# Kernel tuning notes

Hardware: AMD Instinct MI355X
Metric: run time of the kernel (lower is better)

The kernel has to match this reference:

```python
import jax, jax.numpy as jnp
import numpy as np

H = 128
N = 100_000
VOCAB = 15_128
LAYER_TIMESTEPS = [5, 2, 5, 2]
RESIDUALS = {1: [0], 3: [1]}


def gru_cell(x, h, Wih, Whh, bih, bhh):
    # torch.nn.GRUCell semantics
    gi = x @ Wih.T + bih
    gh = h @ Whh.T + bhh
    ir, iz, inn = jnp.split(gi, 3, axis=-1)
    hr, hz, hn = jnp.split(gh, 3, axis=-1)
    r = jax.nn.sigmoid(ir + hr)
    z = jax.nn.sigmoid(iz + hz)
    n = jnp.tanh(inn + r * hn)
    return (1.0 - z) * n + z * h


def setup_inputs() -> dict:
    key = jax.random.key(0)
    ks = jax.random.split(key, 12)
    E_AST, E_MASTER, V, P = 100_000, 20_000, 30_000, 8_000
    s = 1.0 / np.sqrt(H)
    inp = {
        "node_type_ids": jax.random.randint(ks[0], (N,), 0, VOCAB),
        "edges_ast": jax.random.randint(ks[1], (E_AST, 2), 0, N),
        "edges_master": jax.random.randint(ks[2], (E_MASTER, 2), 0, N),
        "var_node_pos": jax.random.randint(ks[3], (V,), 0, N),
        "pred_node_ids": jax.random.randint(ks[4], (P,), 0, N),
        # learned params
        "embedding": jax.random.normal(ks[5], (VOCAB, H), jnp.float32) * 0.02,
        "msg_W": jax.random.normal(ks[6], (4, 4, H, H), jnp.float32) * s,  # [layer, edge_type, H, H]
        "msg_b": jnp.zeros((4, 4, H), jnp.float32),
        "Wih_a": jax.random.normal(ks[7], (2, 3 * H, H), jnp.float32) * s,      # GRU input weights, layers 0,2 (no residual)
        "Wih_b": jax.random.normal(ks[8], (2, 3 * H, 2 * H), jnp.float32) * s,  # layers 1,3 (one residual, concat -> 2H)
        "Whh": jax.random.normal(ks[9], (4, 3 * H, H), jnp.float32) * s,
        "bih": jnp.zeros((4, 3 * H), jnp.float32),
        "bhh": jnp.zeros((4, 3 * H), jnp.float32),
    }
    return inp


def reference(node_type_ids, edges_ast, edges_master, var_node_pos, pred_node_ids,
              embedding, msg_W, msg_b, Wih_a, Wih_b, Whh, bih, bhh):
    # initial node encodings via embedding lookup
    h = embedding[node_type_ids]  # [N, H]
    # 4 edge types: ast, reversed ast, var->master, master->var
    edge_lists = [edges_ast, edges_ast[:, ::-1], edges_master, edges_master[:, ::-1]]
    node_states = [h]
    num_nodes = h.shape[0]
    for layer in range(4):
        res_states = [node_states[l] for l in RESIDUALS.get(layer, [])]
        Wih = Wih_a[layer // 2] if layer in (0, 2) else Wih_b[layer // 2]
        for _ in range(LAYER_TIMESTEPS[layer]):
            incoming = jnp.zeros_like(h)
            for e, edges in enumerate(edge_lists):
                # gather source states, per-edge-type linear, scatter-add to targets
                msg = h[edges[:, 0]] @ msg_W[layer, e].T + msg_b[layer, e]
                incoming = incoming + jax.ops.segment_sum(msg, edges[:, 1], num_segments=num_nodes)
            x = jnp.concatenate([incoming] + res_states, axis=-1) if res_states else incoming
            h = gru_cell(x, h, Wih, Whh[layer], bih[layer], bhh[layer])
        node_states.append(h)
    tree_node_encoding = h
    packed_variable_encoding = tree_node_encoding[var_node_pos]
    prediction_node_encoding = tree_node_encoding[pred_node_ids]
    return tree_node_encoding, packed_variable_encoding, prediction_node_encoding
```

## Files before the change

kernel.cpp:

```cpp
#include <hip/hip_runtime.h>
#include <math.h>

#define H 128
#define NN 100000
#define E_AST 100000
#define E_MST 20000
#define E_TOT 240000
#define NV 30000
#define NP 8000
#define N4 400000
#define NH 12800000
#define VOCAB 15128

typedef unsigned short ushort_t;
typedef __attribute__((ext_vector_type(8))) unsigned short us8;
typedef _Float16 half8 __attribute__((ext_vector_type(8)));
typedef __attribute__((ext_vector_type(4))) float f32x4;

__device__ __forceinline__ unsigned short f2h(float f) {
    _Float16 h = (_Float16)f;
    return __builtin_bit_cast(unsigned short, h);
}
__device__ __forceinline__ float h2f(unsigned short u) {
    return (float)__builtin_bit_cast(_Float16, u);
}
__device__ __forceinline__ void fsplit(float x, unsigned short& hi, unsigned short& lo) {
    _Float16 a = (_Float16)x;
    _Float16 b = (_Float16)(x - (float)a);
    hi = __builtin_bit_cast(unsigned short, a);
    lo = __builtin_bit_cast(unsigned short, b);
}

#define GLD16(gsrc, ldst) __builtin_amdgcn_global_load_lds( \
    (const __attribute__((address_space(1))) unsigned int*)(gsrc), \
    (__attribute__((address_space(3))) unsigned int*)(ldst), 16, 0, 0)

__global__ void embed_kernel(const int* __restrict__ ids, const float* __restrict__ emb,
                             ushort_t* __restrict__ h16, ushort_t* __restrict__ hlo) {
    int g = blockIdx.x * 256 + threadIdx.x;
    if (g >= NN * 64) return;
    int i = g >> 6, j2 = (g & 63) << 1;
    float2 v = *(const float2*)&emb[(size_t)ids[i] * H + j2];
    unsigned short h0, l0, h1, l1;
    fsplit(v.x, h0, l0); fsplit(v.y, h1, l1);
    *(unsigned*)&h16[(size_t)i * H + j2] = (unsigned)h0 | ((unsigned)h1 << 16);
    *(unsigned*)&hlo[(size_t)i * H + j2] = (unsigned)l0 | ((unsigned)l1 << 16);
}

__device__ inline void edge_decode(int t, const int* __restrict__ ast, const int* __restrict__ mst,
                                   int& e, int& src, int& tgt) {
    if (t < E_AST)                 { e = 0; src = ast[2*t];     tgt = ast[2*t+1]; }
    else if (t < 2*E_AST)          { int i = t - E_AST;         e = 1; src = ast[2*i+1]; tgt = ast[2*i]; }
    else if (t < 2*E_AST + E_MST)  { int i = t - 2*E_AST;       e = 2; src = mst[2*i];   tgt = mst[2*i+1]; }
    else                           { int i = t - 2*E_AST-E_MST; e = 3; src = mst[2*i+1]; tgt = mst[2*i]; }
}

__global__ void count4_kernel(const int* __restrict__ ast, const int* __restrict__ mst,
                              int* __restrict__ deg4) {
    int t = blockIdx.x * 256 + threadIdx.x;
    if (t >= E_TOT) return;
    int e, src, tgt; edge_decode(t, ast, mst, e, src, tgt);
    atomicAdd(&deg4[tgt * 4 + e], 1);
}

__global__ void scan1b(const int* __restrict__ deg, int* __restrict__ excl,
                       int* __restrict__ partial, int n) {
    __shared__ int sm[256];
    int t = threadIdx.x, b = blockIdx.x;
    int base = b * 2048 + t * 8;
    int v[8]; int s = 0;
    #pragma unroll
    for (int i = 0; i < 8; ++i) { v[i] = (base + i < n) ? deg[base + i] : 0; s += v[i]; }
    sm[t] = s;
    __syncthreads();
    for (int off = 1; off < 256; off <<= 1) {
        int x = (t >= off) ? sm[t - off] : 0;
        __syncthreads();
        sm[t] += x;
        __syncthreads();
    }
    int run = sm[t] - s;
    if (t == 255) partial[b] = sm[255];
    #pragma unroll
    for (int i = 0; i < 8; ++i) {
        if (base + i < n) { excl[base + i] = run; run += v[i]; }
    }
}

__global__ void scan2(int* __restrict__ partial, int nb) {
    __shared__ int sm[256];
    int t = threadIdx.x;
    int v = (t < nb) ? partial[t] : 0;
    sm[t] = v;
    __syncthreads();
    for (int off = 1; off < 256; off <<= 1) {
        int x = (t >= off) ? sm[t - off] : 0;
        __syncthreads();
        sm[t] += x;
        __syncthreads();
    }
    if (t < nb) partial[t] = sm[t] - v;
}

__global__ void scan3b(int* __restrict__ rp, const int* __restrict__ partial, int n, int etot) {
    int i = blockIdx.x * 256 + threadIdx.x;
    if (i < n) rp[i] += partial[i >> 11];
    if (i == n) rp[n] = etot;
}

__global__ void fill4_kernel(const int* __restrict__ ast, const int* __restrict__ mst,
                             const int* __restrict__ rp4, int* __restrict__ cnt4,
                             int* __restrict__ col) {
    int t = blockIdx.x * 256 + threadIdx.x;
    if (t >= E_TOT) return;
    int e, src, tgt; edge_decode(t, ast, mst, e, src, tgt);
    int key = tgt * 4 + e;
    int slot = rp4[key] + atomicAdd(&cnt4[key], 1);
    col[slot] = src;
}

__global__ void prep_wmsg2(const float* __restrict__ W, ushort_t* __restrict__ hi,
                           ushort_t* __restrict__ lo) {
    int i = blockIdx.x * 256 + threadIdx.x;
    if (i >= 262144) return;
    fsplit(W[i], hi[i], lo[i]);
}

__global__ void prep_emb16(const float* __restrict__ emb, ushort_t* __restrict__ emb16) {
    int i = blockIdx.x * 256 + threadIdx.x;
    if (i >= VOCAB * H) return;
    emb16[i] = f2h(emb[i]);
}

__global__ void prep_B2(const float* __restrict__ Wih_a, const float* __restrict__ Wih_b,
                        const float* __restrict__ Whh,
                        ushort_t* __restrict__ B1h, ushort_t* __restrict__ B1l,
                        ushort_t* __restrict__ B2h, ushort_t* __restrict__ B2l) {
    int i = blockIdx.x * 256 + threadIdx.x;
    if (i >= 327680) return;
    int l, off, K;
    if (i < 65536)       { l = 0; off = 0;      K = 256; }
    else if (i < 163840) { l = 1; off = 65536;  K = 384; }
    else if (i < 229376) { l = 2; off = 163840; K = 256; }
    else                 { l = 3; off = 229376; K = 384; }
    int Kx = K - 128;
    const float* Wih = (l & 1) ? (Wih_b + (size_t)(l >> 1) * 384 * 256)
                               : (Wih_a + (size_t)(l >> 1) * 384 * 128);
    const float* WhhL = Whh + (size_t)l * 384 * 128;
    int rem = i - off;
    int row = rem / K, k = rem - row * K;
    int j = row >> 1, s = row & 1;
    int g1 = s * 128 + j;
    float v1 = (k < Kx) ? Wih[(size_t)g1 * Kx + k] : WhhL[(size_t)g1 * 128 + (k - Kx)];
    fsplit(v1, B1h[i], B1l[i]);
    int g2 = 256 + j;
    float v2;
    if (s == 0) v2 = (k < Kx) ? Wih[(size_t)g2 * Kx + k] : 0.f;
    else        v2 = (k < Kx) ? 0.f : WhhL[(size_t)g2 * 128 + (k - Kx)];
    fsplit(v2, B2h[i], B2l[i]);
}

__global__ __launch_bounds__(256, 4) void msg_gemm(
    const ushort_t* __restrict__ h16, const ushort_t* __restrict__ Whi,
    const ushort_t* __restrict__ Wlo, ushort_t* __restrict__ TA, ushort_t* __restrict__ TB)
{
    __shared__ ushort_t sh[16384];
    ushort_t* Ah = sh;
    ushort_t* Bs = sh + 8192;
    const int tid = threadIdx.x, w = tid >> 6, l = tid & 63;
    const int m0 = blockIdx.x * 128;
    const int n0 = blockIdx.y * 128;
    const int wm = w >> 1, wn = w & 1;
    const int lr8 = l >> 3, lslot = (l & 7) ^ lr8;
    f32x4 acc[4][4];
    #pragma unroll
    for (int a = 0; a < 4; ++a)
        #pragma unroll
        for (int b = 0; b < 4; ++b) acc[a][b] = (f32x4){0.f, 0.f, 0.f, 0.f};

    for (int kt = 0; kt < 2; ++kt) {
        const int kk = kt * 64;
        #pragma unroll
        for (int q = 0; q < 4; ++q) {
            int row8 = w * 4 + q;
            int grow = m0 + row8 * 8 + lr8; if (grow >= NN) grow = NN - 1;
            GLD16(h16 + (size_t)grow * H + kk + lslot * 8, Ah + row8 * 512);
        }
        #pragma unroll
        for (int q = 0; q < 4; ++q) {
            int row8 = w * 4 + q;
            GLD16(Whi + (size_t)(n0 + row8 * 8 + lr8) * 128 + kk + lslot * 8, Bs + row8 * 512);
        }
        __syncthreads();
        #pragma unroll
        for (int fk = 0; fk < 2; ++fk) {
            half8 av[4], bv[4];
            #pragma unroll
            for (int fm = 0; fm < 4; ++fm) {
                int row = wm * 64 + fm * 16 + (l & 15);
                int slot = (fk * 4 + (l >> 4)) ^ (row & 7);
                av[fm] = *(const half8*)&Ah[row * 64 + slot * 8];
            }
            #pragma unroll
            for (int fn = 0; fn < 4; ++fn) {
                int row = wn * 64 + fn * 16 + (l & 15);
                int slot = (fk * 4 + (l >> 4)) ^ (row & 7);
                bv[fn] = *(const half8*)&Bs[row * 64 + slot * 8];
            }
            #pragma unroll
            for (int fm = 0; fm < 4; ++fm)
                #pragma unroll
                for (int fn = 0; fn < 4; ++fn)
                    acc[fm][fn] = __builtin_amdgcn_mfma_f32_16x16x32_f16(av[fm], bv[fn], acc[fm][fn], 0, 0, 0);
        }
        __syncthreads();
        #pragma unroll
        for (int q = 0; q < 4; ++q) {
            int row8 = w * 4 + q;
            GLD16(Wlo + (size_t)(n0 + row8 * 8 + lr8) * 128 + kk + lslot * 8, Bs + row8 * 512);
        }
        __syncthreads();
        #pragma unroll
        for (int fk = 0; fk < 2; ++fk) {
            half8 av[4], bv[4];
            #pragma unroll
            for (int fm = 0; fm < 4; ++fm) {
                int row = wm * 64 + fm * 16 + (l & 15);
                int slot = (fk * 4 + (l >> 4)) ^ (row & 7);
                av[fm] = *(const half8*)&Ah[row * 64 + slot * 8];
            }
            #pragma unroll
            for (int fn = 0; fn < 4; ++fn) {
                int row = wn * 64 + fn * 16 + (l & 15);
                int slot = (fk * 4 + (l >> 4)) ^ (row & 7);
                bv[fn] = *(const half8*)&Bs[row * 64 + slot * 8];
            }
            #pragma unroll
            for (int fm = 0; fm < 4; ++fm)
                #pragma unroll
                for (int fn = 0; fn < 4; ++fn)
                    acc[fm][fn] = __builtin_amdgcn_mfma_f32_16x16x32_f16(av[fm], bv[fn], acc[fm][fn], 0, 0, 0);
        }
        __syncthreads();
    }
    #pragma unroll
    for (int fm = 0; fm < 4; ++fm)
        #pragma unroll
        for (int fn = 0; fn < 4; ++fn) {
            int colL = wn * 64 + fn * 16 + (l & 15);
            #pragma unroll
            for (int rg = 0; rg < 4; ++rg) {
                int rowL = wm * 64 + fm * 16 + (l >> 4) * 4 + rg;
                sh[rowL * 128 + colL] = f2h(acc[fm][fn][rg]);
            }
        }
    __syncthreads();
    {
        int row = tid >> 1, half = tid & 1;
        int grow = m0 + row;
        if (grow < NN) {
            ushort_t* dst = ((blockIdx.y < 2) ? TA : TB) + (size_t)grow * 256 + (blockIdx.y & 1) * 128 + half * 64;
            const ushort_t* src = &sh[row * 128 + half * 64];
            #pragma unroll
            for (int q = 0; q < 8; ++q)
                *(us8*)&dst[q * 8] = *(const us8*)&src[q * 8];
        }
    }
}

__global__ void gather_all(const ushort_t* __restrict__ TA, const ushort_t* __restrict__ TB,
                           const int* __restrict__ rp4, const int* __restrict__ col,
                           const int* __restrict__ deg4, const float* __restrict__ mb,
                           ushort_t* __restrict__ inc16) {
    int wv = threadIdx.x >> 6, l = threadIdx.x & 63;
    int t = blockIdx.x * 4 + wv;
    if (t >= NN) return;
    int c2 = l * 2;
    float a0 = 0.f, a1 = 0.f;
    #pragma unroll
    for (int e4 = 0; e4 < 4; ++e4) {
        float d = (float)deg4[t * 4 + e4];
        a0 += d * mb[e4 * H + c2];
        a1 += d * mb[e4 * H + c2 + 1];
    }
    #pragma unroll
    for (int e = 0; e < 4; ++e) {
        const ushort_t* Tb = (e < 2) ? TA : TB;
        int cb = (e & 1) * 128;
        int s0 = rp4[4 * t + e], s1 = rp4[4 * t + e + 1];
        for (int s = s0; s < s1; ++s) {
            unsigned vv = *(const unsigned*)&Tb[(size_t)col[s] * 256 + cb + c2];
            a0 += h2f((unsigned short)(vv & 0xffff));
            a1 += h2f((unsigned short)(vv >> 16));
        }
    }
    *(unsigned*)&inc16[(size_t)t * H + c2] = (unsigned)f2h(a0) | ((unsigned)f2h(a1) << 16);
}

template<int CFG>
__global__ __launch_bounds__(256, 3) void gru_fused(
    const ushort_t* __restrict__ inc16, ushort_t* __restrict__ h16, ushort_t* __restrict__ hlo,
    const ushort_t* __restrict__ s1h, const ushort_t* __restrict__ emb16, const int* __restrict__ ids,
    const ushort_t* __restrict__ B1h, const ushort_t* __restrict__ B1l,
    const ushort_t* __restrict__ B2h, const ushort_t* __restrict__ B2l,
    const float* __restrict__ bihL, const float* __restrict__ bhhL)
{
    constexpr int NPARTS = (CFG == 0) ? 2 : 3;
    constexpr int K = NPARTS * 128;
    __shared__ ushort_t sh[18432];
    ushort_t* Ah = sh;
    ushort_t* Bs = sh + 2048;
    const int tid = threadIdx.x, w = tid >> 6, l = tid & 63;
    const int m0 = blockIdx.x * 32;
    const int lr8 = l >> 3, lslot = (l & 7) ^ lr8;

    float rzr[2][4][4], rzz[2][4][4];
    f32x4 acc[2][4];

    #pragma unroll
    for (int pass = 0; pass < 2; ++pass) {
        const ushort_t* Bh = pass ? B2h : B1h;
        const ushort_t* Bl = pass ? B2l : B1l;
        #pragma unroll
        for (int a = 0; a < 2; ++a)
            #pragma unroll
            for (int b = 0; b < 4; ++b) acc[a][b] = (f32x4){0.f, 0.f, 0.f, 0.f};

        for (int kt = 0; kt < NPARTS * 2; ++kt) {
            const int p = kt >> 1;
            const int kk = (kt & 1) * 64;
            const int kb = p * 128 + kk;
            {
                int grow = m0 + w * 8 + lr8;
                const ushort_t* sb;
                if (p == 0)               sb = inc16 + (size_t)grow * H;
                else if (p == NPARTS - 1) sb = h16 + (size_t)grow * H;
                else if (CFG == 1)        sb = emb16 + (size_t)ids[grow] * H;
                else                      sb = s1h + (size_t)grow * H;
                GLD16(sb + kk + lslot * 8, Ah + w * 512);
            }
            #pragma unroll
            for (int q = 0; q < 8; ++q)
                GLD16(Bh + (size_t)((w * 8 + q) * 8 + lr8) * K + kb + lslot * 8, Bs + (w * 8 + q) * 512);
            __syncthreads();
            #pragma unroll
            for (int fk = 0; fk < 2; ++fk) {
                half8 av[2], bv[4];
                #pragma unroll
                for (int fm = 0; fm < 2; ++fm) {
                    int row = fm * 16 + (l & 15);
                    int slot = (fk * 4 + (l >> 4)) ^ (row & 7);
                    av[fm] = *(const half8*)&Ah[row * 64 + slot * 8];
                }
                #pragma unroll
                for (int fn = 0; fn < 4; ++fn) {
                    int row = w * 64 + fn * 16 + (l & 15);
                    int slot = (fk * 4 + (l >> 4)) ^ (row & 7);
                    bv[fn] = *(const half8*)&Bs[row * 64 + slot * 8];
                }
                #pragma unroll
                for (int fm = 0; fm < 2; ++fm)
                    #pragma unroll
                    for (int fn = 0; fn < 4; ++fn)
                        acc[fm][fn] = __builtin_amdgcn_mfma_f32_16x16x32_f16(av[fm], bv[fn], acc[fm][fn], 0, 0, 0);
            }
            __syncthreads();
            #pragma unroll
            for (int q = 0; q < 8; ++q)
                GLD16(Bl + (size_t)((w * 8 + q) * 8 + lr8) * K + kb + lslot * 8, Bs + (w * 8 + q) * 512);
            __syncthreads();
            #pragma unroll
            for (int fk = 0; fk < 2; ++fk) {
                half8 av[2], bv[4];
                #pragma unroll
                for (int fm = 0; fm < 2; ++fm) {
                    int row = fm * 16 + (l & 15);
                    int slot = (fk * 4 + (l >> 4)) ^ (row & 7);
                    av[fm] = *(const half8*)&Ah[row * 64 + slot * 8];
                }
                #pragma unroll
                for (int fn = 0; fn < 4; ++fn) {
                    int row = w * 64 + fn * 16 + (l & 15);
                    int slot = (fk * 4 + (l >> 4)) ^ (row & 7);
                    bv[fn] = *(const half8*)&Bs[row * 64 + slot * 8];
                }
                #pragma unroll
                for (int fm = 0; fm < 2; ++fm)
                    #pragma unroll
                    for (int fn = 0; fn < 4; ++fn)
                        acc[fm][fn] = __builtin_amdgcn_mfma_f32_16x16x32_f16(av[fm], bv[fn], acc[fm][fn], 0, 0, 0);
            }
            __syncthreads();
        }

        if (pass == 0) {
            #pragma unroll
            for (int fn = 0; fn < 4; ++fn) {
                int cc = w * 64 + fn * 16 + (l & 15);
                int j = cc >> 1, s = cc & 1;
                float bsum = s ? (bihL[128 + j] + bhhL[128 + j]) : (bihL[j] + bhhL[j]);
                #pragma unroll
                for (int fm = 0; fm < 2; ++fm)
                    #pragma unroll
                    for (int rg = 0; rg < 4; ++rg) {
                        float g = 1.f / (1.f + __expf(-(acc[fm][fn][rg] + bsum)));
                        float other = __shfl_xor(g, 1);
                        rzr[fm][fn][rg] = s ? other : g;
                        rzz[fm][fn][rg] = s ? g : other;
                    }
            }
        } else {
            ushort_t* ohi = Bs;
            ushort_t* olo = Bs + 4096;
            #pragma unroll
            for (int fn = 0; fn < 4; ++fn) {
                int cc = w * 64 + fn * 16 + (l & 15);
                int j = cc >> 1, s = cc & 1;
                float bsum = s ? bhhL[256 + j] : bihL[256 + j];
                #pragma unroll
                for (int fm = 0; fm < 2; ++fm)
                    #pragma unroll
                    for (int rg = 0; rg < 4; ++rg) {
                        float self = acc[fm][fn][rg] + bsum;
                        float other = __shfl_xor(self, 1);
                        if (s == 0) {
                            int rl = fm * 16 + (l >> 4) * 4 + rg;
                            int row = m0 + rl;
                            float n = tanhf(self + rzr[fm][fn][rg] * other);
                            float hold = h2f(h16[(size_t)row * H + j]) + h2f(hlo[(size_t)row * H + j]);
                            float z = rzz[fm][fn][rg];
                            float o = (1.f - z) * n + z * hold;
                            unsigned short hi, lo;
                            fsplit(o, hi, lo);
                            ohi[rl * 128 + j] = hi;
                            olo[rl * 128 + j] = lo;
                        }
                    }
            }
            __syncthreads();
            {
                int row = tid >> 3, seg = tid & 7;
                size_t go = (size_t)(m0 + row) * H + seg * 16;
                *(us8*)&h16[go]     = *(const us8*)&ohi[row * 128 + seg * 16];
                *(us8*)&h16[go + 8] = *(const us8*)&ohi[row * 128 + seg * 16 + 8];
                *(us8*)&hlo[go]     = *(const us8*)&olo[row * 128 + seg * 16];
                *(us8*)&hlo[go + 8] = *(const us8*)&olo[row * 128 + seg * 16 + 8];
            }
        }
    }
}

__global__ void recon_kernel(const ushort_t* __restrict__ h16, const ushort_t* __restrict__ hlo,
                             float* __restrict__ out) {
    int g = blockIdx.x * 256 + threadIdx.x;
    if (g >= NN * 64) return;
    unsigned hi2 = *(const unsigned*)&h16[(size_t)g * 2];
    unsigned lo2 = *(const unsigned*)&hlo[(size_t)g * 2];
    float2 o;
    o.x = h2f((unsigned short)(hi2 & 0xffff)) + h2f((unsigned short)(lo2 & 0xffff));
    o.y = h2f((unsigned short)(hi2 >> 16)) + h2f((unsigned short)(lo2 >> 16));
    *(float2*)&out[(size_t)g * 2] = o;
}

__global__ void out_gather(const float* __restrict__ h, const int* __restrict__ idx,
                           float* __restrict__ out, int n) {
    int g = blockIdx.x * 256 + threadIdx.x;
    if (g >= n * 64) return;
    int v = g >> 6, j2 = (g & 63) << 1;
    *(float2*)&out[(size_t)v * H + j2] = *(const float2*)&h[(size_t)idx[v] * H + j2];
}

extern "C" void kernel_launch(void* const* d_in, const int* in_sizes, int n_in,
                              void* d_out, int out_size, void* d_ws, size_t ws_size,
                              hipStream_t stream) {
    const int*   ids    = (const int*)d_in[0];
    const int*   ast    = (const int*)d_in[1];
    const int*   mst    = (const int*)d_in[2];
    const int*   varpos = (const int*)d_in[3];
    const int*   predid = (const int*)d_in[4];
    const float* emb    = (const float*)d_in[5];
    const float* msg_W  = (const float*)d_in[6];
    const float* msg_b  = (const float*)d_in[7];
    const float* Wih_a  = (const float*)d_in[8];
    const float* Wih_b  = (const float*)d_in[9];
    const float* Whh    = (const float*)d_in[10];
    const float* bih    = (const float*)d_in[11];
    const float* bhh    = (const float*)d_in[12];

    float* out = (float*)d_out;
    ushort_t* TB = (ushort_t*)out;

    int* ibase = (int*)(out + NH);
    int* deg4  = ibase;
    int* rp4   = ibase + 400000;
    int* cnt4  = ibase + 800001;
    int* col   = ibase + 1200001;
    int* part  = ibase + 1440001;
    ushort_t* WT    = (ushort_t*)(ibase + 1500000);
    ushort_t* wmh   = WT;
    ushort_t* wml   = WT + 262144;
    ushort_t* B1h   = WT + 524288;
    ushort_t* B1l   = WT + 851968;
    ushort_t* B2h   = WT + 1179648;
    ushort_t* B2l   = WT + 1507328;
    ushort_t* emb16 = WT + 1835008;

    if (ws_size < (size_t)153600000) return;
    char* wsb = (char*)d_ws;
    ushort_t* h16   = (ushort_t*)wsb;
    ushort_t* hlo   = (ushort_t*)(wsb + 25600000);
    ushort_t* s1h   = (ushort_t*)(wsb + 51200000);
    ushort_t* inc16 = (ushort_t*)(wsb + 76800000);
    ushort_t* TA    = (ushort_t*)(wsb + 102400000);

    embed_kernel<<<25000, 256, 0, stream>>>(ids, emb, h16, hlo);

    hipMemsetAsync(deg4, 0, N4 * sizeof(int), stream);
    hipMemsetAsync(cnt4, 0, N4 * sizeof(int), stream);
    count4_kernel<<<(E_TOT + 255) / 256, 256, 0, stream>>>(ast, mst, deg4);
    scan1b<<<196, 256, 0, stream>>>(deg4, rp4, part, N4);
    scan2<<<1, 256, 0, stream>>>(part, 196);
    scan3b<<<1563, 256, 0, stream>>>(rp4, part, N4, E_TOT);
    fill4_kernel<<<(E_TOT + 255) / 256, 256, 0, stream>>>(ast, mst, rp4, cnt4, col);
    prep_wmsg2<<<1024, 256, 0, stream>>>(msg_W, wmh, wml);
    prep_B2<<<1280, 256, 0, stream>>>(Wih_a, Wih_b, Whh, B1h, B1l, B2h, B2l);
    prep_emb16<<<7564, 256, 0, stream>>>(emb, emb16);

    const int LT[4] = {5, 2, 5, 2};
    const int Boff[4] = {0, 65536, 163840, 229376};
    for (int layer = 0; layer < 4; ++layer) {
        const float* bihL = bih + layer * 384;
        const float* bhhL = bhh + layer * 384;
        const float* mbL  = msg_b + (size_t)layer * 512;
        const ushort_t* wmhL = wmh + (size_t)layer * 65536;
        const ushort_t* wmlL = wml + (size_t)layer * 65536;
        const ushort_t* B1hL = B1h + Boff[layer];
        const ushort_t* B1lL = B1l + Boff[layer];
        const ushort_t* B2hL = B2h + Boff[layer];
        const ushort_t* B2lL = B2l + Boff[layer];

        for (int ts = 0; ts < LT[layer]; ++ts) {
            msg_gemm<<<dim3(782, 4), 256, 0, stream>>>(h16, wmhL, wmlL, TA, TB);
            gather_all<<<25000, 256, 0, stream>>>(TA, TB, rp4, col, deg4, mbL, inc16);
            if (layer == 0 || layer == 2)
                gru_fused<0><<<3125, 256, 0, stream>>>(inc16, h16, hlo, s1h, emb16, ids,
                    B1hL, B1lL, B2hL, B2lL, bihL, bhhL);
            else if (layer == 1)
                gru_fused<1><<<3125, 256, 0, stream>>>(inc16, h16, hlo, s1h, emb16, ids,
                    B1hL, B1lL, B2hL, B2lL, bihL, bhhL);
            else
                gru_fused<2><<<3125, 256, 0, stream>>>(inc16, h16, hlo, s1h, emb16, ids,
                    B1hL, B1lL, B2hL, B2lL, bihL, bhhL);
        }
        if (layer == 0)
            hipMemcpyAsync(s1h, h16, (size_t)NH * 2, hipMemcpyDeviceToDevice, stream);
    }

    recon_kernel<<<25000, 256, 0, stream>>>(h16, hlo, out);
    out_gather<<<(NV * 64 + 255) / 256, 256, 0, stream>>>(out, varpos, out + NH, NV);
    out_gather<<<(NP * 64 + 255) / 256, 256, 0, stream>>>(out, predid, out + NH + (size_t)NV * H, NP);
}
```

Measured before the change: 3.559 ms.

## Load GEMM operands directly from global into registers, dropping LDS staging

The message GEMM and the GRU GEMM now read A and B fragments straight from global memory into registers and feed MFMA, instead of staging tiles in LDS with global_load_lds and block barriers. This removes the LDS round trip and all __syncthreads in the K loop, and the shared-memory footprint of the GRU kernel shrinks. In exchange, operand data shared between waves is re-read from global/L2 by each wave, loads become smaller strided accesses, and register pressure rises, which is why msg_gemm's launch bounds drop from 4 to 3 blocks per CU.

```diff
diff --git a/kernel.cpp b/kernel.cpp
--- a/kernel.cpp
+++ b/kernel.cpp
@@ -30,10 +30,6 @@
     hi = __builtin_bit_cast(unsigned short, a);
     lo = __builtin_bit_cast(unsigned short, b);
 }
-
-#define GLD16(gsrc, ldst) __builtin_amdgcn_global_load_lds( \
-    (const __attribute__((address_space(1))) unsigned int*)(gsrc), \
-    (__attribute__((address_space(3))) unsigned int*)(ldst), 16, 0, 0)
 
 __global__ void embed_kernel(const int* __restrict__ ids, const float* __restrict__ emb,
                              ushort_t* __restrict__ h16, ushort_t* __restrict__ hlo) {
@@ -160,89 +156,54 @@
     fsplit(v2, B2h[i], B2l[i]);
 }
 
-__global__ __launch_bounds__(256, 4) void msg_gemm(
+__global__ __launch_bounds__(256, 3) void msg_gemm(
     const ushort_t* __restrict__ h16, const ushort_t* __restrict__ Whi,
     const ushort_t* __restrict__ Wlo, ushort_t* __restrict__ TA, ushort_t* __restrict__ TB)
 {
     __shared__ ushort_t sh[16384];
-    ushort_t* Ah = sh;
-    ushort_t* Bs = sh + 8192;
     const int tid = threadIdx.x, w = tid >> 6, l = tid & 63;
-    const int m0 = blockIdx.x * 128;
-    const int n0 = blockIdx.y * 128;
+    const int m0 = blockIdx.x * 128, n0 = blockIdx.y * 128;
     const int wm = w >> 1, wn = w & 1;
-    const int lr8 = l >> 3, lslot = (l & 7) ^ lr8;
     f32x4 acc[4][4];
     #pragma unroll
     for (int a = 0; a < 4; ++a)
         #pragma unroll
         for (int b = 0; b < 4; ++b) acc[a][b] = (f32x4){0.f, 0.f, 0.f, 0.f};
 
-    for (int kt = 0; kt < 2; ++kt) {
-        const int kk = kt * 64;
-        #pragma unroll
-        for (int q = 0; q < 4; ++q) {
-            int row8 = w * 4 + q;
-            int grow = m0 + row8 * 8 + lr8; if (grow >= NN) grow = NN - 1;
-            GLD16(h16 + (size_t)grow * H + kk + lslot * 8, Ah + row8 * 512);
-        }
-        #pragma unroll
-        for (int q = 0; q < 4; ++q) {
-            int row8 = w * 4 + q;
-            GLD16(Whi + (size_t)(n0 + row8 * 8 + lr8) * 128 + kk + lslot * 8, Bs + row8 * 512);
-        }
-        __syncthreads();
-        #pragma unroll
-        for (int fk = 0; fk < 2; ++fk) {
-            half8 av[4], bv[4];
-            #pragma unroll
-            for (int fm = 0; fm < 4; ++fm) {
-                int row = wm * 64 + fm * 16 + (l & 15);
-                int slot = (fk * 4 + (l >> 4)) ^ (row & 7);
-                av[fm] = *(const half8*)&Ah[row * 64 + slot * 8];
-            }
+    const ushort_t* abase[4];
+    const ushort_t* bhbase[4];
+    const ushort_t* blbase[4];
+    #pragma unroll
+    for (int fm = 0; fm < 4; ++fm) {
+        int r = m0 + wm * 64 + fm * 16 + (l & 15);
+        if (r >= NN) r = NN - 1;
+        abase[fm] = h16 + (size_t)r * H;
+    }
+    #pragma unroll
+    for (int fn = 0; fn < 4; ++fn) {
+        int r = n0 + wn * 64 + fn * 16 + (l & 15);
+        bhbase[fn] = Whi + (size_t)r * 128;
+        blbase[fn] = Wlo + (size_t)r * 128;
+    }
+
+    #pragma unroll
+    for (int kq = 0; kq < 4; ++kq) {
+        int ko = kq * 32 + (l >> 4) * 8;
+        half8 av[4], bh[4], bl[4];
+        #pragma unroll
+        for (int fm = 0; fm < 4; ++fm) av[fm] = *(const half8*)&abase[fm][ko];
+        #pragma unroll
+        for (int fn = 0; fn < 4; ++fn) { bh[fn] = *(const half8*)&bhbase[fn][ko];
+                                         bl[fn] = *(const half8*)&blbase[fn][ko]; }
+        #pragma unroll
+        for (int fm = 0; fm < 4; ++fm)
             #pragma unroll
             for (int fn = 0; fn < 4; ++fn) {
-                int row = wn * 64 + fn * 16 + (l & 15);
-                int slot = (fk * 4 + (l >> 4)) ^ (row & 7);
-                bv[fn] = *(const half8*)&Bs[row * 64 + slot * 8];
-            }
-            #pragma unroll
-            for (int fm = 0; fm < 4; ++fm)
-                #pragma unroll
-                for (int fn = 0; fn < 4; ++fn)
-                    acc[fm][fn] = __builtin_amdgcn_mfma_f32_16x16x32_f16(av[fm], bv[fn], acc[fm][fn], 0, 0, 0);
-        }
-        __syncthreads();
-        #pragma unroll
-        for (int q = 0; q < 4; ++q) {
-            int row8 = w * 4 + q;
-            GLD16(Wlo + (size_t)(n0 + row8 * 8 + lr8) * 128 + kk + lslot * 8, Bs + row8 * 512);
-        }
-        __syncthreads();
-        #pragma unroll
-        for (int fk = 0; fk < 2; ++fk) {
-            half8 av[4], bv[4];
-            #pragma unroll
-            for (int fm = 0; fm < 4; ++fm) {
-                int row = wm * 64 + fm * 16 + (l & 15);
-                int slot = (fk * 4 + (l >> 4)) ^ (row & 7);
-                av[fm] = *(const half8*)&Ah[row * 64 + slot * 8];
-            }
-            #pragma unroll
-            for (int fn = 0; fn < 4; ++fn) {
-                int row = wn * 64 + fn * 16 + (l & 15);
-                int slot = (fk * 4 + (l >> 4)) ^ (row & 7);
-                bv[fn] = *(const half8*)&Bs[row * 64 + slot * 8];
-            }
-            #pragma unroll
-            for (int fm = 0; fm < 4; ++fm)
-                #pragma unroll
-                for (int fn = 0; fn < 4; ++fn)
-                    acc[fm][fn] = __builtin_amdgcn_mfma_f32_16x16x32_f16(av[fm], bv[fn], acc[fm][fn], 0, 0, 0);
-        }
-        __syncthreads();
-    }
+                acc[fm][fn] = __builtin_amdgcn_mfma_f32_16x16x32_f16(av[fm], bh[fn], acc[fm][fn], 0, 0, 0);
+                acc[fm][fn] = __builtin_amdgcn_mfma_f32_16x16x32_f16(av[fm], bl[fn], acc[fm][fn], 0, 0, 0);
+            }
+    }
+
     #pragma unroll
     for (int fm = 0; fm < 4; ++fm)
         #pragma unroll
@@ -307,12 +268,23 @@
 {
     constexpr int NPARTS = (CFG == 0) ? 2 : 3;
     constexpr int K = NPARTS * 128;
-    __shared__ ushort_t sh[18432];
-    ushort_t* Ah = sh;
-    ushort_t* Bs = sh + 2048;
+    __shared__ ushort_t sh[8192];
     const int tid = threadIdx.x, w = tid >> 6, l = tid & 63;
     const int m0 = blockIdx.x * 32;
-    const int lr8 = l >> 3, lslot = (l & 7) ^ lr8;
+
+    const ushort_t* baseP[NPARTS][2];
+    #pragma unroll
+    for (int fm = 0; fm < 2; ++fm) {
+        int row = m0 + fm * 16 + (l & 15);
+        baseP[0][fm] = inc16 + (size_t)row * H;
+        baseP[NPARTS - 1][fm] = h16 + (size_t)row * H;
+        if (NPARTS == 3)
+            baseP[1][fm] = (CFG == 1) ? emb16 + (size_t)ids[row] * H
+                                      : s1h + (size_t)row * H;
+    }
+    int brow[4];
+    #pragma unroll
+    for (int fn = 0; fn < 4; ++fn) brow[fn] = w * 64 + fn * 16 + (l & 15);
 
     float rzr[2][4][4], rzz[2][4][4];
     f32x4 acc[2][4];
@@ -326,71 +298,26 @@
             #pragma unroll
             for (int b = 0; b < 4; ++b) acc[a][b] = (f32x4){0.f, 0.f, 0.f, 0.f};
 
-        for (int kt = 0; kt < NPARTS * 2; ++kt) {
-            const int p = kt >> 1;
-            const int kk = (kt & 1) * 64;
-            const int kb = p * 128 + kk;
-            {
-                int grow = m0 + w * 8 + lr8;
-                const ushort_t* sb;
-                if (p == 0)               sb = inc16 + (size_t)grow * H;
-                else if (p == NPARTS - 1) sb = h16 + (size_t)grow * H;
-                else if (CFG == 1)        sb = emb16 + (size_t)ids[grow] * H;
-                else                      sb = s1h + (size_t)grow * H;
-                GLD16(sb + kk + lslot * 8, Ah + w * 512);
-            }
-            #pragma unroll
-            for (int q = 0; q < 8; ++q)
-                GLD16(Bh + (size_t)((w * 8 + q) * 8 + lr8) * K + kb + lslot * 8, Bs + (w * 8 + q) * 512);
-            __syncthreads();
-            #pragma unroll
-            for (int fk = 0; fk < 2; ++fk) {
-                half8 av[2], bv[4];
-                #pragma unroll
-                for (int fm = 0; fm < 2; ++fm) {
-                    int row = fm * 16 + (l & 15);
-                    int slot = (fk * 4 + (l >> 4)) ^ (row & 7);
-                    av[fm] = *(const half8*)&Ah[row * 64 + slot * 8];
-                }
+        #pragma unroll
+        for (int kc = 0; kc < NPARTS * 4; ++kc) {
+            const int p = kc >> 2;
+            const int ko = (kc & 3) * 32 + (l >> 4) * 8;
+            const int kob = p * 128 + (kc & 3) * 32 + (l >> 4) * 8;
+            half8 av[2], bh4[4], bl4[4];
+            #pragma unroll
+            for (int fm = 0; fm < 2; ++fm) av[fm] = *(const half8*)&baseP[p][fm][ko];
+            #pragma unroll
+            for (int fn = 0; fn < 4; ++fn) {
+                bh4[fn] = *(const half8*)&Bh[(size_t)brow[fn] * K + kob];
+                bl4[fn] = *(const half8*)&Bl[(size_t)brow[fn] * K + kob];
+            }
+            #pragma unroll
+            for (int fm = 0; fm < 2; ++fm)
                 #pragma unroll
                 for (int fn = 0; fn < 4; ++fn) {
-                    int row = w * 64 + fn * 16 + (l & 15);
-                    int slot = (fk * 4 + (l >> 4)) ^ (row & 7);
-                    bv[fn] = *(const half8*)&Bs[row * 64 + slot * 8];
+                    acc[fm][fn] = __builtin_amdgcn_mfma_f32_16x16x32_f16(av[fm], bh4[fn], acc[fm][fn], 0, 0, 0);
+                    acc[fm][fn] = __builtin_amdgcn_mfma_f32_16x16x32_f16(av[fm], bl4[fn], acc[fm][fn], 0, 0, 0);
                 }
-                #pragma unroll
-                for (int fm = 0; fm < 2; ++fm)
-                    #pragma unroll
-                    for (int fn = 0; fn < 4; ++fn)
-                        acc[fm][fn] = __builtin_amdgcn_mfma_f32_16x16x32_f16(av[fm], bv[fn], acc[fm][fn], 0, 0, 0);
-            }
-            __syncthreads();
-            #pragma unroll
-            for (int q = 0; q < 8; ++q)
-                GLD16(Bl + (size_t)((w * 8 + q) * 8 + lr8) * K + kb + lslot * 8, Bs + (w * 8 + q) * 512);
-            __syncthreads();
-            #pragma unroll
-            for (int fk = 0; fk < 2; ++fk) {
-                half8 av[2], bv[4];
-                #pragma unroll
-                for (int fm = 0; fm < 2; ++fm) {
-                    int row = fm * 16 + (l & 15);
-                    int slot = (fk * 4 + (l >> 4)) ^ (row & 7);
-                    av[fm] = *(const half8*)&Ah[row * 64 + slot * 8];
-                }
-                #pragma unroll
-                for (int fn = 0; fn < 4; ++fn) {
-                    int row = w * 64 + fn * 16 + (l & 15);
-                    int slot = (fk * 4 + (l >> 4)) ^ (row & 7);
-                    bv[fn] = *(const half8*)&Bs[row * 64 + slot * 8];
-                }
-                #pragma unroll
-                for (int fm = 0; fm < 2; ++fm)
-                    #pragma unroll
-                    for (int fn = 0; fn < 4; ++fn)
-                        acc[fm][fn] = __builtin_amdgcn_mfma_f32_16x16x32_f16(av[fm], bv[fn], acc[fm][fn], 0, 0, 0);
-            }
-            __syncthreads();
         }
 
         if (pass == 0) {
@@ -410,8 +337,8 @@
                     }
             }
         } else {
-            ushort_t* ohi = Bs;
-            ushort_t* olo = Bs + 4096;
+            ushort_t* ohi = sh;
+            ushort_t* olo = sh + 4096;
             #pragma unroll
             for (int fn = 0; fn < 4; ++fn) {
                 int cc = w * 64 + fn * 16 + (l & 15);
```

New measurement: 6.398 ms. 1.8x slower.

## Double-buffer weight tiles and stage full A row-block once in GRU GEMM

Applied to the files above, without the earlier changes.

Restructures the fused GRU GEMM kernel so the whole 32-row A block (incoming, residual/embedding, h) is loaded into shared memory once, rather than reloaded for every K tile in both passes. Weight tiles (hi/lo splits of both passes) go into a ping-pong pair of shared buffers, so the next tile loads while the current one is multiplied, with one barrier per unit instead of several. Shared memory grows to roughly 64-88KB, and launch bounds drop from 3 to 2 blocks per CU, which can reduce occupancy and latency hiding.

```diff
diff --git a/kernel.cpp b/kernel.cpp
--- a/kernel.cpp
+++ b/kernel.cpp
@@ -298,7 +298,7 @@
 }
 
 template<int CFG>
-__global__ __launch_bounds__(256, 3) void gru_fused(
+__global__ __launch_bounds__(256, 2) void gru_fused(
     const ushort_t* __restrict__ inc16, ushort_t* __restrict__ h16, ushort_t* __restrict__ hlo,
     const ushort_t* __restrict__ s1h, const ushort_t* __restrict__ emb16, const int* __restrict__ ids,
     const ushort_t* __restrict__ B1h, const ushort_t* __restrict__ B1l,
@@ -307,93 +307,59 @@
 {
     constexpr int NPARTS = (CFG == 0) ? 2 : 3;
     constexpr int K = NPARTS * 128;
-    __shared__ ushort_t sh[18432];
-    ushort_t* Ah = sh;
-    ushort_t* Bs = sh + 2048;
+    constexpr int SLOTS = K / 8;
+    constexpr int AGLD = K / 64;
+    constexpr int NUNITS = NPARTS * 4;
+    __shared__ ushort_t Aall[32 * K];
+    __shared__ ushort_t Bs[2][256 * 64];
     const int tid = threadIdx.x, w = tid >> 6, l = tid & 63;
     const int m0 = blockIdx.x * 32;
-    const int lr8 = l >> 3, lslot = (l & 7) ^ lr8;
+
+    #pragma unroll
+    for (int q = 0; q < AGLD; ++q) {
+        int idx = (w * AGLD + q) * 64 + l;
+        int row = idx / SLOTS;
+        int s   = idx - row * SLOTS;
+        int ss  = s ^ (row & 7);
+        int part = ss >> 4;
+        int grow = m0 + row;
+        const ushort_t* sb;
+        if (part == 0)                sb = inc16 + (size_t)grow * H;
+        else if (part == NPARTS - 1)  sb = h16 + (size_t)grow * H;
+        else                          sb = (CFG == 1) ? emb16 + (size_t)ids[grow] * H
+                                                      : s1h + (size_t)grow * H;
+        GLD16(sb + (ss & 15) * 8, Aall + (size_t)(w * AGLD + q) * 512);
+    }
+
+    #define STAGE_B(Bsel, p_, c_, dstbuf) { \
+        _Pragma("unroll") \
+        for (int q_ = 0; q_ < 8; ++q_) { \
+            int row_ = (w * 8 + q_) * 8 + (l >> 3); \
+            GLD16((Bsel) + (size_t)row_ * K + (p_) * 128 + (c_) * 64 + ((l & 7) ^ (l >> 3)) * 8, \
+                  (dstbuf) + (w * 8 + q_) * 512); \
+        } }
+
+    STAGE_B(B1h, 0, 0, Bs[0]);
+    __syncthreads();
 
     float rzr[2][4][4], rzz[2][4][4];
     f32x4 acc[2][4];
-
-    #pragma unroll
-    for (int pass = 0; pass < 2; ++pass) {
-        const ushort_t* Bh = pass ? B2h : B1h;
-        const ushort_t* Bl = pass ? B2l : B1l;
-        #pragma unroll
-        for (int a = 0; a < 2; ++a)
-            #pragma unroll
-            for (int b = 0; b < 4; ++b) acc[a][b] = (f32x4){0.f, 0.f, 0.f, 0.f};
-
-        for (int kt = 0; kt < NPARTS * 2; ++kt) {
-            const int p = kt >> 1;
-            const int kk = (kt & 1) * 64;
-            const int kb = p * 128 + kk;
-            {
-                int grow = m0 + w * 8 + lr8;
-                const ushort_t* sb;
-                if (p == 0)               sb = inc16 + (size_t)grow * H;
-                else if (p == NPARTS - 1) sb = h16 + (size_t)grow * H;
-                else if (CFG == 1)        sb = emb16 + (size_t)ids[grow] * H;
-                else                      sb = s1h + (size_t)grow * H;
-                GLD16(sb + kk + lslot * 8, Ah + w * 512);
-            }
-            #pragma unroll
-            for (int q = 0; q < 8; ++q)
-                GLD16(Bh + (size_t)((w * 8 + q) * 8 + lr8) * K + kb + lslot * 8, Bs + (w * 8 + q) * 512);
-            __syncthreads();
-            #pragma unroll
-            for (int fk = 0; fk < 2; ++fk) {
-                half8 av[2], bv[4];
-                #pragma unroll
-                for (int fm = 0; fm < 2; ++fm) {
-                    int row = fm * 16 + (l & 15);
-                    int slot = (fk * 4 + (l >> 4)) ^ (row & 7);
-                    av[fm] = *(const half8*)&Ah[row * 64 + slot * 8];
-                }
-                #pragma unroll
-                for (int fn = 0; fn < 4; ++fn) {
-                    int row = w * 64 + fn * 16 + (l & 15);
-                    int slot = (fk * 4 + (l >> 4)) ^ (row & 7);
-                    bv[fn] = *(const half8*)&Bs[row * 64 + slot * 8];
-                }
-                #pragma unroll
-                for (int fm = 0; fm < 2; ++fm)
-                    #pragma unroll
-                    for (int fn = 0; fn < 4; ++fn)
-                        acc[fm][fn] = __builtin_amdgcn_mfma_f32_16x16x32_f16(av[fm], bv[fn], acc[fm][fn], 0, 0, 0);
-            }
-            __syncthreads();
-            #pragma unroll
-            for (int q = 0; q < 8; ++q)
-                GLD16(Bl + (size_t)((w * 8 + q) * 8 + lr8) * K + kb + lslot * 8, Bs + (w * 8 + q) * 512);
-            __syncthreads();
-            #pragma unroll
-            for (int fk = 0; fk < 2; ++fk) {
-                half8 av[2], bv[4];
-                #pragma unroll
-                for (int fm = 0; fm < 2; ++fm) {
-                    int row = fm * 16 + (l & 15);
-                    int slot = (fk * 4 + (l >> 4)) ^ (row & 7);
-                    av[fm] = *(const half8*)&Ah[row * 64 + slot * 8];
-                }
-                #pragma unroll
-                for (int fn = 0; fn < 4; ++fn) {
-                    int row = w * 64 + fn * 16 + (l & 15);
-                    int slot = (fk * 4 + (l >> 4)) ^ (row & 7);
-                    bv[fn] = *(const half8*)&Bs[row * 64 + slot * 8];
-                }
-                #pragma unroll
-                for (int fm = 0; fm < 2; ++fm)
-                    #pragma unroll
-                    for (int fn = 0; fn < 4; ++fn)
-                        acc[fm][fn] = __builtin_amdgcn_mfma_f32_16x16x32_f16(av[fm], bv[fn], acc[fm][fn], 0, 0, 0);
-            }
-            __syncthreads();
-        }
-
-        if (pass == 0) {
+    #pragma unroll
+    for (int a = 0; a < 2; ++a)
+        #pragma unroll
+        for (int b = 0; b < 4; ++b) acc[a][b] = (f32x4){0.f, 0.f, 0.f, 0.f};
+
+    #pragma unroll
+    for (int u = 0; u < 2 * NUNITS; ++u) {
+        if (u + 1 < 2 * NUNITS) {
+            const int un = u + 1;
+            const int pass_n = (un >= NUNITS) ? 1 : 0;
+            const int vn = un - pass_n * NUNITS;
+            const int hl_n = vn & 1, c_n = (vn >> 1) & 1, p_n = vn >> 2;
+            const ushort_t* Bsel = pass_n ? (hl_n ? B2l : B2h) : (hl_n ? B1l : B1h);
+            STAGE_B(Bsel, p_n, c_n, Bs[un & 1]);
+        }
+        if (u == NUNITS) {
             #pragma unroll
             for (int fn = 0; fn < 4; ++fn) {
                 int cc = w * 64 + fn * 16 + (l & 15);
@@ -407,46 +373,75 @@
                         float other = __shfl_xor(g, 1);
                         rzr[fm][fn][rg] = s ? other : g;
                         rzz[fm][fn][rg] = s ? g : other;
+                        acc[fm][fn][rg] = 0.f;
                     }
             }
-        } else {
-            ushort_t* ohi = Bs;
-            ushort_t* olo = Bs + 4096;
-            #pragma unroll
-            for (int fn = 0; fn < 4; ++fn) {
-                int cc = w * 64 + fn * 16 + (l & 15);
-                int j = cc >> 1, s = cc & 1;
-                float bsum = s ? bhhL[256 + j] : bihL[256 + j];
+        }
+        {
+            const int pass = (u >= NUNITS) ? 1 : 0;
+            const int v = u - pass * NUNITS;
+            const int c = (v >> 1) & 1, p = v >> 2;
+            #pragma unroll
+            for (int fk = 0; fk < 2; ++fk) {
+                half8 av[2], bv[4];
+                #pragma unroll
+                for (int fm = 0; fm < 2; ++fm) {
+                    int Ra = fm * 16 + (l & 15);
+                    int slot = (p * 16 + c * 8 + fk * 4 + (l >> 4)) ^ (Ra & 7);
+                    av[fm] = *(const half8*)&Aall[(size_t)Ra * K + slot * 8];
+                }
+                #pragma unroll
+                for (int fn = 0; fn < 4; ++fn) {
+                    int Rb = w * 64 + fn * 16 + (l & 15);
+                    int slot = (fk * 4 + (l >> 4)) ^ (Rb & 7);
+                    bv[fn] = *(const half8*)&Bs[u & 1][(size_t)Rb * 64 + slot * 8];
+                }
                 #pragma unroll
                 for (int fm = 0; fm < 2; ++fm)
                     #pragma unroll
-                    for (int rg = 0; rg < 4; ++rg) {
-                        float self = acc[fm][fn][rg] + bsum;
-                        float other = __shfl_xor(self, 1);
-                        if (s == 0) {
-                            int rl = fm * 16 + (l >> 4) * 4 + rg;
-                            int row = m0 + rl;
-                            float n = tanhf(self + rzr[fm][fn][rg] * other);
-                            float hold = h2f(h16[(size_t)row * H + j]) + h2f(hlo[(size_t)row * H + j]);
-                            float z = rzz[fm][fn][rg];
-                            float o = (1.f - z) * n + z * hold;
-                            unsigned short hi, lo;
-                            fsplit(o, hi, lo);
-                            ohi[rl * 128 + j] = hi;
-                            olo[rl * 128 + j] = lo;
-                        }
-                    }
-            }
-            __syncthreads();
-            {
-                int row = tid >> 3, seg = tid & 7;
-                size_t go = (size_t)(m0 + row) * H + seg * 16;
-                *(us8*)&h16[go]     = *(const us8*)&ohi[row * 128 + seg * 16];
-                *(us8*)&h16[go + 8] = *(const us8*)&ohi[row * 128 + seg * 16 + 8];
-                *(us8*)&hlo[go]     = *(const us8*)&olo[row * 128 + seg * 16];
-                *(us8*)&hlo[go + 8] = *(const us8*)&olo[row * 128 + seg * 16 + 8];
-            }
-        }
+                    for (int fn = 0; fn < 4; ++fn)
+                        acc[fm][fn] = __builtin_amdgcn_mfma_f32_16x16x32_f16(av[fm], bv[fn], acc[fm][fn], 0, 0, 0);
+            }
+        }
+        __syncthreads();
+    }
+    #undef STAGE_B
+
+    ushort_t* ohi = Bs[0];
+    ushort_t* olo = Bs[0] + 4096;
+    #pragma unroll
+    for (int fn = 0; fn < 4; ++fn) {
+        int cc = w * 64 + fn * 16 + (l & 15);
+        int j = cc >> 1, s = cc & 1;
+        float bsum = s ? bhhL[256 + j] : bihL[256 + j];
+        #pragma unroll
+        for (int fm = 0; fm < 2; ++fm)
+            #pragma unroll
+            for (int rg = 0; rg < 4; ++rg) {
+                float self = acc[fm][fn][rg] + bsum;
+                float other = __shfl_xor(self, 1);
+                if (s == 0) {
+                    int rl = fm * 16 + (l >> 4) * 4 + rg;
+                    int row = m0 + rl;
+                    float n = tanhf(self + rzr[fm][fn][rg] * other);
+                    float hold = h2f(h16[(size_t)row * H + j]) + h2f(hlo[(size_t)row * H + j]);
+                    float z = rzz[fm][fn][rg];
+                    float o = (1.f - z) * n + z * hold;
+                    unsigned short hi, lo;
+                    fsplit(o, hi, lo);
+                    ohi[rl * 128 + j] = hi;
+                    olo[rl * 128 + j] = lo;
+                }
+            }
+    }
+    __syncthreads();
+    {
+        int row = tid >> 3, seg = tid & 7;
+        size_t go = (size_t)(m0 + row) * H + seg * 16;
+        *(us8*)&h16[go]     = *(const us8*)&ohi[row * 128 + seg * 16];
+        *(us8*)&h16[go + 8] = *(const us8*)&ohi[row * 128 + seg * 16 + 8];
+        *(us8*)&hlo[go]     = *(const us8*)&olo[row * 128 + seg * 16];
+        *(us8*)&hlo[go + 8] = *(const us8*)&olo[row * 128 + seg * 16 + 8];
     }
 }
 
```

Measured after the change: 4.416 ms. 24.1% more time.
